# Performance work log

Measured on AMD Instinct MI355X. Metric: run time of the kernel, lower is better.

## Reference

```python
import jax, jax.numpy as jnp
import numpy as np

N_NODES = 59392        # batch_size * node_each_graph = 512 * 116
N_EDGES = 1187840      # avg degree 20

def _graph_conv(h, src, dst, W, b, out_norm, in_norm):
    # DGL GraphConv, norm='both': act((D_in^-1/2 A D_out^-1/2 h) W + b)
    h = h * out_norm[:, None]
    m = jax.ops.segment_sum(h[src], dst, num_segments=N_NODES)  # sparse aggregation
    m = m * in_norm[:, None]
    return jax.nn.relu(m @ W + b)

def setup_inputs() -> dict:
    key = jax.random.key(0)
    ks = jax.random.split(key, 8)
    feat = jax.random.normal(ks[0], (N_NODES, 116), dtype=jnp.float32)
    src = jax.random.randint(ks[1], (N_EDGES,), 0, N_NODES)
    dst = jax.random.randint(ks[2], (N_EDGES,), 0, N_NODES)
    W1 = jax.random.normal(ks[3], (116, 64), dtype=jnp.float32) * 0.05
    b1 = jnp.zeros((64,), dtype=jnp.float32)
    W2 = jax.random.normal(ks[4], (64, 64), dtype=jnp.float32) * 0.05
    b2 = jnp.zeros((64,), dtype=jnp.float32)
    Wc = jax.random.normal(ks[5], (116 * 64, 2), dtype=jnp.float32) * 0.05
    bc = jnp.zeros((2,), dtype=jnp.float32)
    return {"feat": feat, "src": src, "dst": dst, "batch_size": 512,
            "W1": W1, "b1": b1, "W2": W2, "b2": b2, "Wc": Wc, "bc": bc}

def reference(feat, src, dst, batch_size, W1, b1, W2, b2, Wc, bc):
    ones = jnp.ones((N_EDGES,), dtype=jnp.float32)
    out_deg = jax.ops.segment_sum(ones, src, num_segments=N_NODES)
    in_deg = jax.ops.segment_sum(ones, dst, num_segments=N_NODES)
    out_norm = jax.lax.rsqrt(jnp.maximum(out_deg, 1.0))
    in_norm = jax.lax.rsqrt(jnp.maximum(in_deg, 1.0))
    h = _graph_conv(feat, src, dst, W1, b1, out_norm, in_norm)
    # dropout is identity in eval mode
    h = _graph_conv(h, src, dst, W2, b2, out_norm, in_norm)
    h = h.reshape(batch_size, -1)  # (B, node_each_graph * hid)
    return h @ Wc + bc
```

## Files before the change

kernel.cpp:

```cpp
#include <hip/hip_runtime.h>

#define N_NODES 59392
#define N_EDGES 1187840
#define F_IN 116
#define F_HID 64
#define BATCH 512
#define NPG 116
#define CCAP 64
#define NSLD 160
#define EPSD (N_EDGES / NSLD)
#define NSLS 64
#define EPSS (N_EDGES / NSLS)
#define NR 4
#define NPR4 (N_NODES / NR)
#define GPB 4
#define NPB (NPG / GPB)

typedef __attribute__((ext_vector_type(8))) short short8;
typedef __attribute__((ext_vector_type(4))) float float4v;

__device__ __forceinline__ float u2f(unsigned u) {
    union { unsigned u; float f; } x; x.u = u; return x.f;
}
__device__ __forceinline__ float bf2f(unsigned short h) {
    union { unsigned u; float f; } x; x.u = (unsigned)h << 16; return x.f;
}
__device__ __forceinline__ unsigned short f2bf(float f) {
    union { float f; unsigned u; } x; x.f = f;
    unsigned r = x.u + 0x7FFF + ((x.u >> 16) & 1);
    return (unsigned short)(r >> 16);
}

__global__ __launch_bounds__(256) void hist_kernel(const int* __restrict__ src,
                                                   const int* __restrict__ dst,
                                                   unsigned short* __restrict__ cnt2,
                                                   unsigned short* __restrict__ cnt2s) {
    __shared__ unsigned bins[NPR4 / 2];
    int tid = threadIdx.x;
    int b = blockIdx.x;
    const int* __restrict__ idx;
    unsigned short* outp;
    int slice, range, nedge;
    if (b < NSLD * NR) {
        slice = b >> 2; range = b & 3; idx = dst; outp = cnt2; nedge = EPSD;
    } else {
        int bb = b - NSLD * NR;
        slice = bb >> 2; range = bb & 3; idx = src; outp = cnt2s; nedge = EPSS;
    }
    int r0 = range * NPR4;
    long ebase = (long)slice * nedge;
    for (int k = tid; k < NPR4 / 2; k += 256) bins[k] = 0;
    __syncthreads();
    for (int k = tid; k < nedge; k += 256) {
        int v = idx[ebase + k] - r0;
        if ((unsigned)v < NPR4) atomicAdd(&bins[v >> 1], 1u << ((v & 1) * 16));
    }
    __syncthreads();
    unsigned* op = (unsigned*)(outp + (size_t)slice * N_NODES + r0);
    for (int k = tid; k < NPR4 / 2; k += 256) op[k] = bins[k];
}

__global__ __launch_bounds__(256) void scan_norm_kernel(unsigned short* __restrict__ cnt2,
                                                        const unsigned short* __restrict__ cnt2s,
                                                        float* __restrict__ onorm,
                                                        float* __restrict__ inorm,
                                                        int* __restrict__ ncnt) {
    int d = blockIdx.x * 256 + threadIdx.x;
    int run = 0;
    for (int i = 0; i < NSLD; ++i) {
        size_t ix = (size_t)i * N_NODES + d;
        int c = cnt2[ix];
        cnt2[ix] = (unsigned short)run;
        run += c;
    }
    int o = 0;
    for (int i = 0; i < NSLS; ++i) o += cnt2s[(size_t)i * N_NODES + d];
    onorm[d] = rsqrtf(fmaxf((float)o, 1.0f));
    inorm[d] = rsqrtf(fmaxf((float)run, 1.0f));
    ncnt[d] = run < CCAP ? run : CCAP;
}

__global__ __launch_bounds__(256) void gemm1_kernel(const float* __restrict__ feat,
                                                    const float* __restrict__ W1,
                                                    const float* __restrict__ onorm,
                                                    unsigned short* __restrict__ A1h) {
    int lane = threadIdx.x & 63;
    int c16 = lane & 15, quad = lane >> 4;
    short8 Bhi[4][4], Blo[4][4];
    #pragma unroll
    for (int kiter = 0; kiter < 4; ++kiter) {
        #pragma unroll
        for (int t = 0; t < 4; ++t) {
            #pragma unroll
            for (int j = 0; j < 8; ++j) {
                int k = kiter * 32 + quad * 8 + j;
                float w = (k < F_IN) ? W1[k * F_HID + t * 16 + c16] : 0.f;
                unsigned short hi = f2bf(w);
                unsigned short lo = f2bf(w - bf2f(hi));
                Bhi[kiter][t][j] = (short)hi;
                Blo[kiter][t][j] = (short)lo;
            }
        }
    }
    int wid = (blockIdx.x * 256 + threadIdx.x) >> 6;
    int nwaves = (gridDim.x * 256) >> 6;
    const int ntiles = N_NODES / 16;
    for (int tile = wid; tile < ntiles; tile += nwaves) {
        int base = tile * 16;
        int row = base + c16;
        float on = onorm[row];
        const float* fp = feat + (size_t)row * F_IN;
        float4v acc[4] = {{0.f,0.f,0.f,0.f},{0.f,0.f,0.f,0.f},{0.f,0.f,0.f,0.f},{0.f,0.f,0.f,0.f}};
        #pragma unroll
        for (int kiter = 0; kiter < 4; ++kiter) {
            int koff = kiter * 32 + quad * 8;
            float f[8];
            if (koff + 8 <= F_IN) {
                float4 x = *(const float4*)(fp + koff);
                float4 y = *(const float4*)(fp + koff + 4);
                f[0]=x.x; f[1]=x.y; f[2]=x.z; f[3]=x.w;
                f[4]=y.x; f[5]=y.y; f[6]=y.z; f[7]=y.w;
            } else {
                #pragma unroll
                for (int j = 0; j < 8; ++j) f[j] = (koff + j < F_IN) ? fp[koff + j] : 0.f;
            }
            short8 ah, al;
            #pragma unroll
            for (int j = 0; j < 8; ++j) {
                float v = f[j] * on;
                unsigned short hi = f2bf(v);
                ah[j] = (short)hi;
                al[j] = (short)f2bf(v - bf2f(hi));
            }
            #pragma unroll
            for (int t = 0; t < 4; ++t) {
                acc[t] = __builtin_amdgcn_mfma_f32_16x16x32_bf16(ah, Bhi[kiter][t], acc[t], 0, 0, 0);
                acc[t] = __builtin_amdgcn_mfma_f32_16x16x32_bf16(al, Bhi[kiter][t], acc[t], 0, 0, 0);
                acc[t] = __builtin_amdgcn_mfma_f32_16x16x32_bf16(ah, Blo[kiter][t], acc[t], 0, 0, 0);
            }
        }
        #pragma unroll
        for (int t = 0; t < 4; ++t) {
            #pragma unroll
            for (int r = 0; r < 4; ++r) {
                int node = base + quad * 4 + r;
                A1h[(size_t)node * F_HID + t * 16 + c16] = f2bf(acc[t][r]);
            }
        }
    }
}

__global__ __launch_bounds__(256) void place_kernel(const int* __restrict__ src,
                                                    const int* __restrict__ dst,
                                                    const unsigned short* __restrict__ cnt2,
                                                    unsigned short* __restrict__ ebuf) {
    __shared__ unsigned cur[NPR4 / 2];
    int tid = threadIdx.x;
    int slice = blockIdx.x >> 2;
    int r0 = (blockIdx.x & 3) * NPR4;
    long ebase = (long)slice * EPSD;
    const unsigned* pp = (const unsigned*)(cnt2 + (size_t)slice * N_NODES + r0);
    for (int k = tid; k < NPR4 / 2; k += 256) cur[k] = pp[k];
    __syncthreads();
    #pragma unroll 1
    for (int t = 0; t < 7; ++t) {
        int k = t * 1024 + tid;
        int d0 = dst[ebase + k],        s0 = src[ebase + k];
        int d1 = dst[ebase + k + 256],  s1 = src[ebase + k + 256];
        int d2 = dst[ebase + k + 512],  s2 = src[ebase + k + 512];
        int d3 = dst[ebase + k + 768],  s3 = src[ebase + k + 768];
        #define PLACE1(dd, ss)                                                    \
            { int dr = (dd) - r0;                                                 \
              if ((unsigned)dr < NPR4) {                                          \
                  int sh = (dr & 1) * 16;                                         \
                  unsigned old = atomicAdd(&cur[dr >> 1], 1u << sh);              \
                  unsigned pos = (old >> sh) & 0xFFFFu;                           \
                  if (pos < CCAP) ebuf[(size_t)(dd) * CCAP + pos] = (unsigned short)(ss); } }
        PLACE1(d0, s0) PLACE1(d1, s1) PLACE1(d2, s2) PLACE1(d3, s3)
    }
    {
        int k = 7168 + tid;
        int d0 = dst[ebase + k], s0 = src[ebase + k];
        PLACE1(d0, s0)
        #undef PLACE1
    }
}

#define GATHER_PRE(BASE, N, A0, A1, A2, A3)                                       \
    {                                                                             \
        unsigned long long ch[8], rw[8];                                          \
        _Pragma("unroll")                                                         \
        for (int t = 0; t < 8; ++t) ch[t] = ebq[t];                               \
        int id[8];                                                                \
        _Pragma("unroll")                                                         \
        for (int t = 0; t < 8; ++t)                                               \
            id[t] = (t * 4 + g4 < (N)) ? (int)((ch[t] >> sh16) & 0xFFFFu) : 0;    \
        _Pragma("unroll")                                                         \
        for (int t = 0; t < 8; ++t)                                               \
            rw[t] = *(const unsigned long long*)((BASE) + id[t] * 32 + c16 * 2);  \
        _Pragma("unroll")                                                         \
        for (int t = 0; t < 8; ++t) {                                             \
            unsigned lo = (unsigned)rw[t], hi = (unsigned)(rw[t] >> 32);          \
            if (t * 4 + g4 >= (N)) { lo = 0u; hi = 0u; }                          \
            A0 += u2f(lo << 16); A1 += u2f(lo & 0xFFFF0000u);                     \
            A2 += u2f(hi << 16); A3 += u2f(hi & 0xFFFF0000u);                     \
        }                                                                         \
        int nq = ((N) + 3) >> 2;                                                  \
        for (int t = 8; t < nq; ++t) {                          \
            unsigned long long c = ebq[t];                                        \
            int e = t * 4 + g4;                                                   \
            int ix = (e < (N)) ? (int)((c >> sh16) & 0xFFFFu) : 0;                \
            unsigned long long w = *(const unsigned long long*)((BASE) + ix * 32 + c16 * 2); \
            unsigned lo = (unsigned)w, hi = (unsigned)(w >> 32);                  \
            if (e >= (N)) { lo = 0u; hi = 0u; }                                   \
            A0 += u2f(lo << 16); A1 += u2f(lo & 0xFFFF0000u);                     \
            A2 += u2f(hi << 16); A3 += u2f(hi & 0xFFFF0000u);                     \
        }                                                                         \
        A0 += __shfl_xor(A0, 16); A1 += __shfl_xor(A1, 16);                       \
        A2 += __shfl_xor(A2, 16); A3 += __shfl_xor(A3, 16);                       \
        A0 += __shfl_xor(A0, 32); A1 += __shfl_xor(A1, 32);                       \
        A2 += __shfl_xor(A2, 32); A3 += __shfl_xor(A3, 32);                       \
    }

__global__ __launch_bounds__(256) void gather1_kernel(const int* __restrict__ ncnt,
                                                      const unsigned short* __restrict__ ebuf,
                                                      const unsigned short* __restrict__ A1h,
                                                      const float* __restrict__ onorm,
                                                      const float* __restrict__ inorm,
                                                      const float* __restrict__ b1,
                                                      unsigned short* __restrict__ H1h) {
    int wave = threadIdx.x >> 6, lane = threadIdx.x & 63;
    int v = blockIdx.x * 4 + wave;
    int c16 = lane & 15, g4 = lane >> 4, sh16 = g4 * 16;
    int n = ncnt[v];
    const unsigned long long* ebq = (const unsigned long long*)(ebuf + (size_t)v * CCAP);
    const unsigned* base = (const unsigned*)A1h;
    float4 b1q = ((const float4*)b1)[c16];
    float in_v = inorm[v], on_v = onorm[v];
    float a0 = 0.f, a1 = 0.f, a2 = 0.f, a3 = 0.f;
    GATHER_PRE(base, n, a0, a1, a2, a3);
    float h0 = fmaxf(in_v * a0 + b1q.x, 0.f) * on_v;
    float h1 = fmaxf(in_v * a1 + b1q.y, 0.f) * on_v;
    float h2 = fmaxf(in_v * a2 + b1q.z, 0.f) * on_v;
    float h3 = fmaxf(in_v * a3 + b1q.w, 0.f) * on_v;
    if (g4 == 0) {
        unsigned lo = (unsigned)f2bf(h0) | ((unsigned)f2bf(h1) << 16);
        unsigned hi = (unsigned)f2bf(h2) | ((unsigned)f2bf(h3) << 16);
        ((unsigned long long*)H1h)[(size_t)v * 16 + c16] =
            ((unsigned long long)hi << 32) | lo;
    }
}

__global__ __launch_bounds__(256) void readout_kernel(const int* __restrict__ ncnt,
                                                      const unsigned short* __restrict__ ebuf,
                                                      const unsigned short* __restrict__ H1h,
                                                      const float* __restrict__ inorm,
                                                      const float* __restrict__ b2,
                                                      const float* __restrict__ W2,
                                                      const float* __restrict__ Wc,
                                                      const float* __restrict__ bc,
                                                      float* __restrict__ out) {
    __shared__ float Gs[NPB][F_HID];
    __shared__ float ls[8];
    int g = blockIdx.x >> 2, part = blockIdx.x & 3;
    int nbase = g * NPG + part * NPB;
    int wave = threadIdx.x >> 6, lane = threadIdx.x & 63;
    int c16 = lane & 15, g4 = lane >> 4, sh16 = g4 * 16;
    const unsigned* base = (const unsigned*)H1h;
    for (int nl = wave; nl < NPB; nl += 4) {
        int v = nbase + nl;
        int n = ncnt[v];
        const unsigned long long* ebq = (const unsigned long long*)(ebuf + (size_t)v * CCAP);
        float a0 = 0.f, a1 = 0.f, a2 = 0.f, a3 = 0.f;
        GATHER_PRE(base, n, a0, a1, a2, a3);
        if (g4 == 0) {
            float4 m4; m4.x = a0; m4.y = a1; m4.z = a2; m4.w = a3;
            *(float4*)&Gs[nl][c16 * 4] = m4;
        }
    }
    __syncthreads();
    float w2[F_HID];
    #pragma unroll
    for (int k = 0; k < F_HID; ++k) w2[k] = W2[k * F_HID + lane];
    float b2l = b2[lane];
    float s0 = 0.f, s1 = 0.f;
    for (int nl = wave; nl < NPB; nl += 4) {
        int v = nbase + nl;
        float acc = 0.f;
        #pragma unroll
        for (int k = 0; k < F_HID; k += 4) {
            float4 gk = *(const float4*)&Gs[nl][k];
            acc += gk.x * w2[k] + gk.y * w2[k + 1] + gk.z * w2[k + 2] + gk.w * w2[k + 3];
        }
        float h = fmaxf(inorm[v] * acc + b2l, 0.f);
        float2 w = ((const float2*)Wc)[(part * NPB + nl) * F_HID + lane];
        s0 += h * w.x;
        s1 += h * w.y;
    }
    #pragma unroll
    for (int off = 32; off > 0; off >>= 1) {
        s0 += __shfl_down(s0, off);
        s1 += __shfl_down(s1, off);
    }
    if (lane == 0) { ls[wave * 2] = s0; ls[wave * 2 + 1] = s1; }
    __syncthreads();
    if (threadIdx.x < 2) {
        float t = 0.f;
        #pragma unroll
        for (int w = 0; w < 4; ++w) t += ls[w * 2 + threadIdx.x];
        if (part == 0) t += bc[threadIdx.x];
        atomicAdd(&out[g * 2 + threadIdx.x], t);
    }
}

extern "C" void kernel_launch(void* const* d_in, const int* in_sizes, int n_in,
                              void* d_out, int out_size, void* d_ws, size_t ws_size,
                              hipStream_t stream) {
    const float* feat = (const float*)d_in[0];
    const int*   src  = (const int*)d_in[1];
    const int*   dst  = (const int*)d_in[2];
    const float* W1 = (const float*)d_in[4];
    const float* b1 = (const float*)d_in[5];
    const float* W2 = (const float*)d_in[6];
    const float* b2 = (const float*)d_in[7];
    const float* Wc = (const float*)d_in[8];
    const float* bc = (const float*)d_in[9];
    float* out = (float*)d_out;

    unsigned short* cnt2  = (unsigned short*)d_ws;
    unsigned short* cnt2s = cnt2 + (size_t)NSLD * N_NODES;
    float* onorm = (float*)(cnt2s + (size_t)NSLS * N_NODES);
    float* inorm = onorm + N_NODES;
    int* ncnt    = (int*)(inorm + N_NODES);
    unsigned short* ebuf = (unsigned short*)(ncnt + N_NODES);
    unsigned short* A1h  = ebuf + (size_t)N_NODES * CCAP;
    unsigned short* H1h  = cnt2;

    hipMemsetAsync(out, 0, (size_t)BATCH * 2 * sizeof(float), stream);
    hist_kernel<<<NSLD * NR + NSLS * NR, 256, 0, stream>>>(src, dst, cnt2, cnt2s);
    scan_norm_kernel<<<N_NODES / 256, 256, 0, stream>>>(cnt2, cnt2s, onorm, inorm, ncnt);
    gemm1_kernel<<<464, 256, 0, stream>>>(feat, W1, onorm, A1h);
    place_kernel<<<NSLD * NR, 256, 0, stream>>>(src, dst, cnt2, ebuf);
    gather1_kernel<<<N_NODES / 4, 256, 0, stream>>>(ncnt, ebuf, A1h, onorm, inorm, b1, H1h);
    readout_kernel<<<BATCH * GPB, 256, 0, stream>>>(ncnt, ebuf, H1h, inorm, b2, W2, Wc, bc, out);
}
```

Before: 226.0 us.

## Fuse scan/norm with GEMM1 and move source-norm scaling into gather

The degree scan/normalisation and the first dense GEMM now run in a single launch. Scan blocks and GEMM blocks are split by block index, which is possible because the GEMM no longer scales by out-norm. That scaling moves into the first gather, which loads onorm per neighbour. Padded neighbour slots point at a sentinel node whose feature row and onorm are zeroed, which removes the masking branches. The output memset is folded into gather1. Together this removes two launches and lets the scan overlap the GEMM, at the cost of an extra per-edge onorm load in gather1 and a layout shift for the sentinel.

```diff
diff --git a/kernel.cpp b/kernel.cpp
--- a/kernel.cpp
+++ b/kernel.cpp
@@ -15,6 +15,8 @@
 #define NPR4 (N_NODES / NR)
 #define GPB 4
 #define NPB (NPG / GPB)
+#define SCAN_BLK (N_NODES / 256)
+#define GEMM_BLK 640
 
 typedef __attribute__((ext_vector_type(8))) short short8;
 typedef __attribute__((ext_vector_type(4))) float float4v;
@@ -60,30 +62,31 @@
     for (int k = tid; k < NPR4 / 2; k += 256) op[k] = bins[k];
 }
 
-__global__ __launch_bounds__(256) void scan_norm_kernel(unsigned short* __restrict__ cnt2,
-                                                        const unsigned short* __restrict__ cnt2s,
-                                                        float* __restrict__ onorm,
-                                                        float* __restrict__ inorm,
-                                                        int* __restrict__ ncnt) {
-    int d = blockIdx.x * 256 + threadIdx.x;
-    int run = 0;
-    for (int i = 0; i < NSLD; ++i) {
-        size_t ix = (size_t)i * N_NODES + d;
-        int c = cnt2[ix];
-        cnt2[ix] = (unsigned short)run;
-        run += c;
-    }
-    int o = 0;
-    for (int i = 0; i < NSLS; ++i) o += cnt2s[(size_t)i * N_NODES + d];
-    onorm[d] = rsqrtf(fmaxf((float)o, 1.0f));
-    inorm[d] = rsqrtf(fmaxf((float)run, 1.0f));
-    ncnt[d] = run < CCAP ? run : CCAP;
-}
-
-__global__ __launch_bounds__(256) void gemm1_kernel(const float* __restrict__ feat,
-                                                    const float* __restrict__ W1,
-                                                    const float* __restrict__ onorm,
-                                                    unsigned short* __restrict__ A1h) {
+__global__ __launch_bounds__(256) void scan_gemm1_kernel(unsigned short* __restrict__ cnt2,
+                                                         const unsigned short* __restrict__ cnt2s,
+                                                         float* __restrict__ onorm,
+                                                         float* __restrict__ inorm,
+                                                         int* __restrict__ ncnt,
+                                                         const float* __restrict__ feat,
+                                                         const float* __restrict__ W1,
+                                                         unsigned short* __restrict__ A1h) {
+    if (blockIdx.x < SCAN_BLK) {
+        int d = blockIdx.x * 256 + threadIdx.x;
+        int run = 0;
+        for (int i = 0; i < NSLD; ++i) {
+            size_t ix = (size_t)i * N_NODES + d;
+            int c = cnt2[ix];
+            cnt2[ix] = (unsigned short)run;
+            run += c;
+        }
+        int o = 0;
+        for (int i = 0; i < NSLS; ++i) o += cnt2s[(size_t)i * N_NODES + d];
+        onorm[d] = rsqrtf(fmaxf((float)o, 1.0f));
+        inorm[d] = rsqrtf(fmaxf((float)run, 1.0f));
+        ncnt[d] = run < CCAP ? run : CCAP;
+        if (d == 0) onorm[N_NODES] = 0.f;
+        return;
+    }
     int lane = threadIdx.x & 63;
     int c16 = lane & 15, quad = lane >> 4;
     short8 Bhi[4][4], Blo[4][4];
@@ -102,13 +105,13 @@
             }
         }
     }
-    int wid = (blockIdx.x * 256 + threadIdx.x) >> 6;
-    int nwaves = (gridDim.x * 256) >> 6;
+    int bid = blockIdx.x - SCAN_BLK;
+    int wid = (bid * 256 + threadIdx.x) >> 6;
+    int nwaves = (GEMM_BLK * 256) >> 6;
     const int ntiles = N_NODES / 16;
     for (int tile = wid; tile < ntiles; tile += nwaves) {
         int base = tile * 16;
         int row = base + c16;
-        float on = onorm[row];
         const float* fp = feat + (size_t)row * F_IN;
         float4v acc[4] = {{0.f,0.f,0.f,0.f},{0.f,0.f,0.f,0.f},{0.f,0.f,0.f,0.f},{0.f,0.f,0.f,0.f}};
         #pragma unroll
@@ -127,7 +130,7 @@
             short8 ah, al;
             #pragma unroll
             for (int j = 0; j < 8; ++j) {
-                float v = f[j] * on;
+                float v = f[j];
                 unsigned short hi = f2bf(v);
                 ah[j] = (short)hi;
                 al[j] = (short)f2bf(v - bf2f(hi));
@@ -186,33 +189,69 @@
     }
 }
 
-#define GATHER_PRE(BASE, N, A0, A1, A2, A3)                                       \
+#define GATHER_ON(BASE, N, A0, A1, A2, A3)                                        \
     {                                                                             \
         unsigned long long ch[8], rw[8];                                          \
+        float onu[8];                                                             \
+        int id[8];                                                                \
         _Pragma("unroll")                                                         \
         for (int t = 0; t < 8; ++t) ch[t] = ebq[t];                               \
-        int id[8];                                                                \
         _Pragma("unroll")                                                         \
         for (int t = 0; t < 8; ++t)                                               \
-            id[t] = (t * 4 + g4 < (N)) ? (int)((ch[t] >> sh16) & 0xFFFFu) : 0;    \
-        _Pragma("unroll")                                                         \
-        for (int t = 0; t < 8; ++t)                                               \
+            id[t] = (t * 4 + g4 < (N)) ? (int)((ch[t] >> sh16) & 0xFFFFu) : N_NODES; \
+        _Pragma("unroll")                                                         \
+        for (int t = 0; t < 8; ++t) {                                             \
             rw[t] = *(const unsigned long long*)((BASE) + id[t] * 32 + c16 * 2);  \
+            onu[t] = onorm[id[t]];                                                \
+        }                                                                         \
         _Pragma("unroll")                                                         \
         for (int t = 0; t < 8; ++t) {                                             \
             unsigned lo = (unsigned)rw[t], hi = (unsigned)(rw[t] >> 32);          \
-            if (t * 4 + g4 >= (N)) { lo = 0u; hi = 0u; }                          \
-            A0 += u2f(lo << 16); A1 += u2f(lo & 0xFFFF0000u);                     \
-            A2 += u2f(hi << 16); A3 += u2f(hi & 0xFFFF0000u);                     \
+            A0 += onu[t] * u2f(lo << 16); A1 += onu[t] * u2f(lo & 0xFFFF0000u);   \
+            A2 += onu[t] * u2f(hi << 16); A3 += onu[t] * u2f(hi & 0xFFFF0000u);   \
         }                                                                         \
         int nq = ((N) + 3) >> 2;                                                  \
         for (int t = 8; t < nq; ++t) {                          \
             unsigned long long c = ebq[t];                                        \
             int e = t * 4 + g4;                                                   \
-            int ix = (e < (N)) ? (int)((c >> sh16) & 0xFFFFu) : 0;                \
+            int ix = (e < (N)) ? (int)((c >> sh16) & 0xFFFFu) : N_NODES;          \
+            unsigned long long w = *(const unsigned long long*)((BASE) + ix * 32 + c16 * 2); \
+            float ou = onorm[ix];                                                 \
+            unsigned lo = (unsigned)w, hi = (unsigned)(w >> 32);                  \
+            A0 += ou * u2f(lo << 16); A1 += ou * u2f(lo & 0xFFFF0000u);           \
+            A2 += ou * u2f(hi << 16); A3 += ou * u2f(hi & 0xFFFF0000u);           \
+        }                                                                         \
+        A0 += __shfl_xor(A0, 16); A1 += __shfl_xor(A1, 16);                       \
+        A2 += __shfl_xor(A2, 16); A3 += __shfl_xor(A3, 16);                       \
+        A0 += __shfl_xor(A0, 32); A1 += __shfl_xor(A1, 32);                       \
+        A2 += __shfl_xor(A2, 32); A3 += __shfl_xor(A3, 32);                       \
+    }
+
+#define GATHER_Z(BASE, N, A0, A1, A2, A3)                                         \
+    {                                                                             \
+        unsigned long long ch[8], rw[8];                                          \
+        int id[8];                                                                \
+        _Pragma("unroll")                                                         \
+        for (int t = 0; t < 8; ++t) ch[t] = ebq[t];                               \
+        _Pragma("unroll")                                                         \
+        for (int t = 0; t < 8; ++t)                                               \
+            id[t] = (t * 4 + g4 < (N)) ? (int)((ch[t] >> sh16) & 0xFFFFu) : N_NODES; \
+        _Pragma("unroll")                                                         \
+        for (int t = 0; t < 8; ++t)                                               \
+            rw[t] = *(const unsigned long long*)((BASE) + id[t] * 32 + c16 * 2);  \
+        _Pragma("unroll")                                                         \
+        for (int t = 0; t < 8; ++t) {                                             \
+            unsigned lo = (unsigned)rw[t], hi = (unsigned)(rw[t] >> 32);          \
+            A0 += u2f(lo << 16); A1 += u2f(lo & 0xFFFF0000u);                     \
+            A2 += u2f(hi << 16); A3 += u2f(hi & 0xFFFF0000u);                     \
+        }                                                                         \
+        int nq = ((N) + 3) >> 2;                                                  \
+        for (int t = 8; t < nq; ++t) {                                            \
+            unsigned long long c = ebq[t];                                        \
+            int e = t * 4 + g4;                                                   \
+            int ix = (e < (N)) ? (int)((c >> sh16) & 0xFFFFu) : N_NODES;          \
             unsigned long long w = *(const unsigned long long*)((BASE) + ix * 32 + c16 * 2); \
             unsigned lo = (unsigned)w, hi = (unsigned)(w >> 32);                  \
-            if (e >= (N)) { lo = 0u; hi = 0u; }                                   \
             A0 += u2f(lo << 16); A1 += u2f(lo & 0xFFFF0000u);                     \
             A2 += u2f(hi << 16); A3 += u2f(hi & 0xFFFF0000u);                     \
         }                                                                         \
@@ -228,7 +267,13 @@
                                                       const float* __restrict__ onorm,
                                                       const float* __restrict__ inorm,
                                                       const float* __restrict__ b1,
-                                                      unsigned short* __restrict__ H1h) {
+                                                      unsigned short* __restrict__ H1h,
+                                                      float* __restrict__ out) {
+    if (blockIdx.x == 0) {
+        int t = threadIdx.x;
+        for (int k = t; k < BATCH * 2; k += 256) out[k] = 0.f;
+        if (t < 16) ((unsigned long long*)(H1h + (size_t)N_NODES * F_HID))[t] = 0ull;
+    }
     int wave = threadIdx.x >> 6, lane = threadIdx.x & 63;
     int v = blockIdx.x * 4 + wave;
     int c16 = lane & 15, g4 = lane >> 4, sh16 = g4 * 16;
@@ -238,7 +283,7 @@
     float4 b1q = ((const float4*)b1)[c16];
     float in_v = inorm[v], on_v = onorm[v];
     float a0 = 0.f, a1 = 0.f, a2 = 0.f, a3 = 0.f;
-    GATHER_PRE(base, n, a0, a1, a2, a3);
+    GATHER_ON(base, n, a0, a1, a2, a3);
     float h0 = fmaxf(in_v * a0 + b1q.x, 0.f) * on_v;
     float h1 = fmaxf(in_v * a1 + b1q.y, 0.f) * on_v;
     float h2 = fmaxf(in_v * a2 + b1q.z, 0.f) * on_v;
@@ -272,7 +317,7 @@
         int n = ncnt[v];
         const unsigned long long* ebq = (const unsigned long long*)(ebuf + (size_t)v * CCAP);
         float a0 = 0.f, a1 = 0.f, a2 = 0.f, a3 = 0.f;
-        GATHER_PRE(base, n, a0, a1, a2, a3);
+        GATHER_Z(base, n, a0, a1, a2, a3);
         if (g4 == 0) {
             float4 m4; m4.x = a0; m4.y = a1; m4.z = a2; m4.w = a3;
             *(float4*)&Gs[nl][c16 * 4] = m4;
@@ -330,17 +375,16 @@
     unsigned short* cnt2  = (unsigned short*)d_ws;
     unsigned short* cnt2s = cnt2 + (size_t)NSLD * N_NODES;
     float* onorm = (float*)(cnt2s + (size_t)NSLS * N_NODES);
-    float* inorm = onorm + N_NODES;
+    float* inorm = onorm + N_NODES + 1;
     int* ncnt    = (int*)(inorm + N_NODES);
     unsigned short* ebuf = (unsigned short*)(ncnt + N_NODES);
     unsigned short* A1h  = ebuf + (size_t)N_NODES * CCAP;
     unsigned short* H1h  = cnt2;
 
-    hipMemsetAsync(out, 0, (size_t)BATCH * 2 * sizeof(float), stream);
     hist_kernel<<<NSLD * NR + NSLS * NR, 256, 0, stream>>>(src, dst, cnt2, cnt2s);
-    scan_norm_kernel<<<N_NODES / 256, 256, 0, stream>>>(cnt2, cnt2s, onorm, inorm, ncnt);
-    gemm1_kernel<<<464, 256, 0, stream>>>(feat, W1, onorm, A1h);
+    scan_gemm1_kernel<<<SCAN_BLK + GEMM_BLK, 256, 0, stream>>>(cnt2, cnt2s, onorm, inorm,
+                                                               ncnt, feat, W1, A1h);
     place_kernel<<<NSLD * NR, 256, 0, stream>>>(src, dst, cnt2, ebuf);
-    gather1_kernel<<<N_NODES / 4, 256, 0, stream>>>(ncnt, ebuf, A1h, onorm, inorm, b1, H1h);
+    gather1_kernel<<<N_NODES / 4, 256, 0, stream>>>(ncnt, ebuf, A1h, onorm, inorm, b1, H1h, out);
     readout_kernel<<<BATCH * GPB, 256, 0, stream>>>(ncnt, ebuf, H1h, inorm, b2, W2, Wc, bc, out);
 }
```

New measurement: 230.8 us. 2.1% more time.
